# Optimization experiments

Hardware: AMD Instinct MI355X
Metric: run time of the kernel (lower is better)

The kernel has to match this reference:

```python
import jax, jax.numpy as jnp
import numpy as np
from jax import lax

D_MODEL = 1024
EXPAND = 2
D_INNER = EXPAND * D_MODEL          # 2048
HEADDIM = 64
NHEADS = D_INNER // HEADDIM         # 32
D_STATE = 128
D_CONV = 4
NGROUPS = 1
CONV_DIM = D_INNER + 2 * NGROUPS * D_STATE   # 2304
D_IN_PROJ = 2 * D_INNER + 2 * NGROUPS * D_STATE + NHEADS  # 4384
EPS = 1e-5
BSZ, SEQ = 4, 1024


def _layer_norm(x):
    mu = jnp.mean(x, -1, keepdims=True)
    v = jnp.var(x, -1, keepdims=True)
    return (x - mu) * lax.rsqrt(v + EPS)


def _smart_flip(X, mask):
    # reverse only the non-padded prefix of each sequence
    B, L, _ = X.shape
    lengths = jnp.sum(~mask, axis=1)                     # (B,)
    r = jnp.arange(L)[None, :]                           # (1,L)
    pos = jnp.where(r < lengths[:, None], lengths[:, None] - 1 - r, r)
    return jnp.take_along_axis(X, pos[:, :, None], axis=1)


def _mamba2(u, in_proj_w, conv_w, conv_b, dt_bias, A_log, D, norm_w, out_proj_w):
    B, L, _ = u.shape
    zxbcdt = jnp.einsum('bld,ed->ble', u, in_proj_w)     # (B,L,D_IN_PROJ)
    z = zxbcdt[..., :D_INNER]
    xBC = zxbcdt[..., D_INNER:D_INNER + CONV_DIM]
    dt = zxbcdt[..., D_INNER + CONV_DIM:]                # (B,L,H)
    dt = jax.nn.softplus(dt + dt_bias)
    # causal depthwise conv1d over time, then SiLU
    xc = jnp.transpose(xBC, (0, 2, 1))                   # (B,C,L)
    xc = jnp.pad(xc, ((0, 0), (0, 0), (D_CONV - 1, 0)))
    xc = lax.conv_general_dilated(xc, conv_w.reshape(CONV_DIM, 1, D_CONV), (1,), 'VALID',
                                  feature_group_count=CONV_DIM)
    xBC = jax.nn.silu(jnp.transpose(xc + conv_b[None, :, None], (0, 2, 1)))
    x = xBC[..., :D_INNER].reshape(B, L, NHEADS, HEADDIM)
    Bmat = xBC[..., D_INNER:D_INNER + D_STATE]           # (B,L,N)  (ngroups=1)
    Cmat = xBC[..., D_INNER + D_STATE:]                  # (B,L,N)
    A = -jnp.exp(A_log)                                  # (H,)
    dA = jnp.exp(dt * A)                                 # (B,L,H)

    def step(h, inp):
        dA_t, dt_t, x_t, B_t, C_t = inp
        # h: (B,H,P,N)
        h = h * dA_t[:, :, None, None] + (dt_t[:, :, None] * x_t)[..., None] * B_t[:, None, None, :]
        y = jnp.einsum('bhpn,bn->bhp', h, C_t)
        return h, y

    h0 = jnp.zeros((B, NHEADS, HEADDIM, D_STATE), u.dtype)
    xs = (jnp.moveaxis(dA, 1, 0), jnp.moveaxis(dt, 1, 0), jnp.moveaxis(x, 1, 0),
          jnp.moveaxis(Bmat, 1, 0), jnp.moveaxis(Cmat, 1, 0))
    _, ys = lax.scan(step, h0, xs)                       # (L,B,H,P)
    y = jnp.moveaxis(ys, 0, 1) + D[None, None, :, None] * x
    y = y.reshape(B, L, D_INNER)
    g = y * jax.nn.silu(z)                               # gated RMSNorm (norm_before_gate=False)
    y = g * lax.rsqrt(jnp.mean(g * g, -1, keepdims=True) + EPS) * norm_w
    return jnp.einsum('ble,de->bld', y, out_proj_w)


def setup_inputs() -> dict:
    key = jax.random.key(0)
    ks = jax.random.split(key, 16)
    dt_f = jax.random.uniform(ks[4], (NHEADS,), minval=0.001, maxval=0.1)
    dt_r = jax.random.uniform(ks[10], (NHEADS,), minval=0.001, maxval=0.1)
    inv_softplus = lambda d: d + jnp.log(-jnp.expm1(-d))
    return {
        'hidden_states': jax.random.normal(ks[0], (BSZ, SEQ, D_MODEL), jnp.float32),
        'src_key_padding_mask': jnp.zeros((BSZ, SEQ), jnp.bool_),
        'in_proj_w': jax.random.normal(ks[1], (D_IN_PROJ, D_MODEL), jnp.float32) / np.sqrt(D_MODEL),
        'out_proj_w': jax.random.normal(ks[2], (D_MODEL, D_INNER), jnp.float32) / np.sqrt(D_INNER),
        'conv_w_f': jax.random.normal(ks[3], (CONV_DIM, D_CONV), jnp.float32) / np.sqrt(D_CONV),
        'conv_b_f': jnp.zeros((CONV_DIM,), jnp.float32),
        'dt_bias_f': inv_softplus(dt_f),
        'A_log_f': jnp.log(jax.random.uniform(ks[5], (NHEADS,), minval=1.0, maxval=16.0)),
        'D_f': jnp.ones((NHEADS,), jnp.float32),
        'norm_w_f': jnp.ones((D_INNER,), jnp.float32),
        'conv_w_r': jax.random.normal(ks[9], (CONV_DIM, D_CONV), jnp.float32) / np.sqrt(D_CONV),
        'conv_b_r': jnp.zeros((CONV_DIM,), jnp.float32),
        'dt_bias_r': inv_softplus(dt_r),
        'A_log_r': jnp.log(jax.random.uniform(ks[11], (NHEADS,), minval=1.0, maxval=16.0)),
        'D_r': jnp.ones((NHEADS,), jnp.float32),
        'norm_w_r': jnp.ones((D_INNER,), jnp.float32),
    }


def reference(hidden_states, src_key_padding_mask, in_proj_w, out_proj_w,
              conv_w_f, conv_b_f, dt_bias_f, A_log_f, D_f, norm_w_f,
              conv_w_r, conv_b_r, dt_bias_r, A_log_r, D_r, norm_w_r):
    h = _layer_norm(hidden_states)
    out = _mamba2(h, in_proj_w, conv_w_f, conv_b_f, dt_bias_f, A_log_f, D_f, norm_w_f, out_proj_w)
    rev = _smart_flip(h, src_key_padding_mask)
    out_rev = _mamba2(rev, in_proj_w, conv_w_r, conv_b_r, dt_bias_r, A_log_r, D_r, norm_w_r, out_proj_w)
    out_rev = _smart_flip(out_rev, src_key_padding_mask)
    out = (out + out_rev) / 2
    return _layer_norm(out)
```

## Files before the change

### kernel.cpp

```cpp
#include <hip/hip_runtime.h>


#define BSZ 4
#define SEQ 1024
#define DMODEL 1024
#define DINNER 2048
#define NHEADS 32
#define HEADDIM 64
#define DSTATE 128
#define CONVDIM 2304
#define DPROJ 4384
#define DPROJ_PAD 4480
#define NTOK (BSZ*SEQ)
#define EPSF 1e-5f
#define CH 32
#define NCHK (SEQ/CH)

typedef float f32x4 __attribute__((ext_vector_type(4)));
typedef __bf16 bf16x8 __attribute__((ext_vector_type(8)));

__device__ __forceinline__ unsigned short f2bf(float f) {
  unsigned int x = __float_as_uint(f);
  unsigned int r = (x + 0x7fffu + ((x >> 16) & 1u)) >> 16;
  return (unsigned short)r;
}
__device__ __forceinline__ float bf2f(unsigned short u) {
  return __uint_as_float(((unsigned int)u) << 16);
}

__device__ __forceinline__ void async_load16(const void* g, void* l) {
  __builtin_amdgcn_global_load_lds(
      (const __attribute__((address_space(1))) void*)g,
      (__attribute__((address_space(3))) void*)l, 16, 0, 0);
}

#define W1N (DPROJ_PAD * DMODEL)
#define W2N (DMODEL * DINNER)
__global__ void k_convert(const float* __restrict__ w1, const float* __restrict__ w2,
                          unsigned short* __restrict__ o1, unsigned short* __restrict__ o2) {
  int idx = blockIdx.x * 256 + threadIdx.x;
  if (idx < W1N) {
    int row = idx >> 10, col = idx & 1023;
    float v = (row < DPROJ) ? w1[(size_t)row * DMODEL + col] : 0.f;
    o1[idx] = f2bf(v);
  } else {
    int k = idx - W1N;
    o2[k] = f2bf(w2[k]);
  }
}
__global__ void k_lengths(const unsigned char* __restrict__ mask, int* __restrict__ lengths) {
  int b = blockIdx.x, tid = threadIdx.x;
  int cnt = 0;
  for (int k = 0; k < 4; ++k)
    cnt += (mask[(size_t)b * SEQ + tid + k * 256] == 0) ? 1 : 0;
  for (int o = 32; o > 0; o >>= 1) cnt += __shfl_down(cnt, o);
  __shared__ int red[4];
  if ((tid & 63) == 0) red[tid >> 6] = cnt;
  __syncthreads();
  if (tid == 0) lengths[b] = red[0] + red[1] + red[2] + red[3];
}

__global__ __launch_bounds__(256) void k_ln_bf16(const float* __restrict__ in,
                                                 unsigned short* __restrict__ out) {
  int row = blockIdx.x, tid = threadIdx.x;
  float4 v = ((const float4*)(in + (size_t)row * DMODEL))[tid];
  float s = v.x + v.y + v.z + v.w;
  float ss = v.x * v.x + v.y * v.y + v.z * v.z + v.w * v.w;
  for (int o = 32; o > 0; o >>= 1) { s += __shfl_down(s, o); ss += __shfl_down(ss, o); }
  __shared__ float red[8];
  if ((tid & 63) == 0) { red[tid >> 6] = s; red[4 + (tid >> 6)] = ss; }
  __syncthreads();
  s = red[0] + red[1] + red[2] + red[3];
// ... 118 lines not shown
  for (int k = 0; k < 9; ++k) {
    int c = tid + k * 256;
    float4 w4 = *(const float4*)(cw + (size_t)c * 4);
    w0[k] = w4.x; w1[k] = w4.y; w2[k] = w4.z; w3[k] = w4.w;
    bias[k] = cb[c];
    r0[k] = 0.f; r1[k] = 0.f; r2[k] = 0.f;
  }
  auto rowptr = [&](int tt) -> const __bf16* {
    int s = dir ? ((tt < len) ? (len - 1 - tt) : tt) : tt;
    return zxb + ((size_t)b * SEQ + s) * DPROJ_PAD + DINNER;
  };
  if (t0 >= 3) {
    const __bf16* ra = rowptr(t0 - 3);
    const __bf16* rb = rowptr(t0 - 2);
    const __bf16* rc = rowptr(t0 - 1);
#pragma unroll
    for (int k = 0; k < 9; ++k) {
      int c = tid + k * 256;
      r0[k] = (float)ra[c]; r1[k] = (float)rb[c]; r2[k] = (float)rc[c];
    }
  }
  {
    const __bf16* rp = rowptr(t0);
#pragma unroll
    for (int k = 0; k < 9; ++k) r3[k] = (float)rp[tid + k * 256];
  }
  for (int j = 0; j < 16; ++j) {
    float r4[9];
    if (j < 15) {
      const __bf16* rp = rowptr(t0 + j + 1);
#pragma unroll
      for (int k = 0; k < 9; ++k) r4[k] = (float)rp[tid + k * 256];
    }
    __bf16* orow = xb + ((size_t)db * SEQ + t0 + j) * CONVDIM;
#pragma unroll
    for (int k = 0; k < 9; ++k) {
      float acc = bias[k];
      acc = fmaf(w0[k], r0[k], acc);
      acc = fmaf(w1[k], r1[k], acc);
      acc = fmaf(w2[k], r2[k], acc);
      acc = fmaf(w3[k], r3[k], acc);
      float sig = 1.f / (1.f + __expf(-acc));
      orow[tid + k * 256] = (__bf16)(acc * sig);
      r0[k] = r1[k]; r1[k] = r2[k]; r2[k] = r3[k]; r3[k] = r4[k];
    }
  }
}

__global__ __launch_bounds__(256) void k_dtprep(
    const __bf16* __restrict__ zxb,
    const float* __restrict__ dtb_f, const float* __restrict__ dtb_r,
    const float* __restrict__ al_f, const float* __restrict__ al_r,
    const int* __restrict__ lengths, float* __restrict__ ddg) {
  const int task = (blockIdx.x * 256 + threadIdx.x) >> 5;
  const int l32 = threadIdx.x & 31;
  const int chunk = task & 31, hh = (task >> 5) & 31, db = task >> 10;
  const int b = db & 3, dir = db >> 2;
  const int len = lengths[b];
  const float dtbv = (dir ? dtb_r : dtb_f)[hh];
  const float Ah = -__expf((dir ? al_r : al_f)[hh]);
  const int s = chunk * 32 + l32;
  const int sf = dir ? ((s < len) ? (len - 1 - s) : s) : s;
  float raw = (float)zxb[(size_t)(b * SEQ + sf) * DPROJ_PAD + DINNER + CONVDIM + hh] + dtbv;
  float d = (raw > 20.f) ? raw : log1pf(__expf(raw));
  float cum = d;
#pragma unroll
  for (int o = 1; o < 32; o <<= 1) {
    float v = __shfl_up(cum, o, 32);
    if (l32 >= o) cum += v;
  }
  float cum31 = __shfl(cum, 31, 32);
  float* o = ddg + (size_t)task * 128;
  o[l32]      = d;
  o[32 + l32] = Ah * cum;
  o[64 + l32] = d * __expf(Ah * (cum31 - cum));
  o[96 + l32] = __expf(Ah * cum);
}

__global__ __launch_bounds__(256, 2) void k_scan(
    const __bf16* __restrict__ xb, const float* __restrict__ ddg,
    const float* __restrict__ D_f, const float* __restrict__ D_r,
    unsigned short* __restrict__ y) {
  __shared__ __bf16 Crawf[4096];
  __shared__ __bf16 Brawf[4096];
  __shared__ __bf16 Braw2[4096];
  __shared__ __bf16 BTf[4096];
  __shared__ float  ddL[2][128];
  __shared__ __bf16 SL[1024];
  __shared__ __bf16 HL[4][2048];
  __shared__ __bf16 yO[2][32 * 72];

  const int bx = blockIdx.x;
  const int h = bx & 31;
  const int db = bx >> 5;
  const int dir = db >> 2;
  const int tid = threadIdx.x;
  const int lane = tid & 63;
  const int w = tid >> 6;
  const int l15 = lane & 15;
  const int q = lane >> 4;

  const float Dh = (dir ? D_r : D_f)[h];
  const __bf16* xbase = xb + (size_t)db * SEQ * CONVDIM;
  const float* ddbase = ddg + (size_t)bx * NCHK * 128;
  unsigned short* ybase = y + (size_t)db * SEQ * DINNER + h * HEADDIM;

  for (int i = lane; i < 2048; i += 64) HL[w][i] = (__bf16)0.f;
  for (int i = tid; i < 1024; i += 256) SL[i] = (__bf16)0.f;

  f32x4 accH[8] = {};

  auto issue = [&](int c, int nb) {
    const __bf16* xr = xbase + (size_t)c * CH * CONVDIM;
#pragma unroll
    for (int k = 0; k < 2; ++k) {
      const int idx = w * 2 + k;
      const int P = idx * 64 + lane;
      const int tt = P >> 8, kk = (P >> 6) & 3, qq = (P >> 4) & 3, ll = P & 15;
      const __bf16* gB = xr + (size_t)(tt * 16 + ll) * CONVDIM + DINNER + kk * 32 + qq * 8;
      async_load16(gB, &Brawf[idx * 512]);
      async_load16(gB + 128, &Crawf[idx * 512]);
      const int s = P >> 4, n8 = P & 15;
      const __bf16* g2 = xr + (size_t)s * CONVDIM + DINNER + n8 * 8;
      async_load16(g2, &Braw2[idx * 512]);
    }
    if (w == 3 && lane < 32)
      async_load16(ddbase + (size_t)c * 128 + lane * 4, &ddL[nb][0]);
  };

  auto load_xt = [&](int c) {
    bf16x8 v;
    const __bf16* gx = xbase + (size_t)(c * CH + q * 8) * CONVDIM + h * HEADDIM + w * 16 + l15;
#pragma unroll
    for (int j = 0; j < 8; ++j) v[j] = gx[(size_t)j * CONVDIM];
    return v;
  };

  issue(0, 0);
  bf16x8 xt = load_xt(0);
  __syncthreads();

  for (int c = 0; c < NCHK; ++c) {
    const int cb = c & 1, nb = cb ^ 1;

    if (c > 0) {
      const int tf = tid >> 3, p8 = (tid & 7) * 8;
      bf16x8 vy = *(const bf16x8*)&yO[nb][tf * 72 + p8];
      *(bf16x8*)(ybase + (size_t)((c - 1) * CH + tf) * DINNER + p8) = vy;
    }

    {
      const int n = tid & 127, sg = tid >> 7;
#pragma unroll
      for (int e = 0; e < 2; ++e) {
        const int qp = sg * 2 + e;
        bf16x8 v;
#pragma unroll
        for (int j = 0; j < 8; ++j) v[j] = Braw2[(qp * 8 + j) * 128 + n];
        *(bf16x8*)&BTf[((n >> 4) * 64 + qp * 16 + (n & 15)) * 8] = v;
      }
    }

    bf16x8 Cf0[4], Cf1[4];
#pragma unroll
    for (int kk = 0; kk < 4; ++kk) {
      Cf0[kk] = *(const bf16x8*)&Crawf[(kk * 64 + lane) * 8];
      Cf1[kk] = *(const bf16x8*)&Crawf[((4 + kk) * 64 + lane) * 8];
    }
    if (w < 3) {
      const int tt = (w == 0) ? 0 : 1;
      const int ss = (w == 2) ? 1 : 0;
      f32x4 G = {};
#pragma unroll
      for (int kk = 0; kk < 4; ++kk) {
        bf16x8 Bq = *(const bf16x8*)&Brawf[((ss * 4 + kk) * 64 + lane) * 8];
        G = __builtin_amdgcn_mfma_f32_16x16x32_bf16(tt ? Cf1[kk] : Cf0[kk], Bq, G, 0, 0, 0);
      }
      const int sgl = ss * 16 + l15;
      const float sdt = ddL[cb][sgl];
      const float scd = ddL[cb][32 + sgl];
#pragma unroll
      for (int r = 0; r < 4; ++r) {
        const int t0 = q * 4 + r;
        float v = G[r] * sdt * __expf(ddL[cb][32 + tt * 16 + t0] - scd);
        if (tt == ss) {
          if (t0 < l15) v = 0.f;
          else if (t0 == l15) v += Dh;
        }
        SL[(tt * 64 + (ss * 2 + (l15 >> 3)) * 16 + t0) * 8 + (l15 & 7)] = (__bf16)v;
      }
    }
    __syncthreads();

    if (c + 1 < NCHK) issue(c + 1, nb);
    bf16x8 xt_n;
    if (c + 1 < NCHK) xt_n = load_xt(c + 1);

    f32x4 accy0 = {}, accy1 = {};
    {
      bf16x8 S0 = *(const bf16x8*)&SL[(lane) * 8];
      bf16x8 S1 = *(const bf16x8*)&SL[(64 + lane) * 8];
      accy0 = __builtin_amdgcn_mfma_f32_16x16x32_bf16(xt, S0, accy0, 0, 0, 0);
      accy1 = __builtin_amdgcn_mfma_f32_16x16x32_bf16(xt, S1, accy1, 0, 0, 0);
    }
    {
      f32x4 ai0 = {}, ai1 = {};
#pragma unroll
      for (int kk = 0; kk < 4; ++kk) {
        bf16x8 Hf = *(const bf16x8*)&HL[w][(kk * 64 + lane) * 8];
        ai0 = __builtin_amdgcn_mfma_f32_16x16x32_bf16(Hf, Cf0[kk], ai0, 0, 0, 0);
        ai1 = __builtin_amdgcn_mfma_f32_16x16x32_bf16(Hf, Cf1[kk], ai1, 0, 0, 0);
      }
      const float P0 = ddL[cb][96 + l15], P1 = ddL[cb][96 + 16 + l15];
      accy0 = accy0 + ai0 * P0;
      accy1 = accy1 + ai1 * P1;
    }
    {
      const float atot = ddL[cb][96 + 31];
      bf16x8 xw;
#pragma unroll
      for (int j = 0; j < 8; ++j)
        xw[j] = (__bf16)((float)xt[j] * ddL[cb][64 + q * 8 + j]);
#pragma unroll
      for (int nt = 0; nt < 8; ++nt) {
        bf16x8 Bt = *(const bf16x8*)&BTf[(nt * 64 + lane) * 8];
        accH[nt] = accH[nt] * atot;
        accH[nt] = __builtin_amdgcn_mfma_f32_16x16x32_bf16(xw, Bt, accH[nt], 0, 0, 0);
      }
#pragma unroll
      for (int nt = 0; nt < 8; ++nt)
#pragma unroll
        for (int r = 0; r < 4; ++r) {
          const int n = nt * 16 + l15;
          HL[w][((n >> 5) * 64 + ((n & 31) >> 3) * 16 + q * 4 + r) * 8 + (n & 7)] =
              (__bf16)accH[nt][r];
        }
    }
#pragma unroll
    for (int r = 0; r < 4; ++r) {
      const int p = w * 16 + q * 4 + r;
      yO[cb][l15 * 72 + p]        = (__bf16)accy0[r];
      yO[cb][(16 + l15) * 72 + p] = (__bf16)accy1[r];
    }
    xt = xt_n;
    __syncthreads();
  }
  {
    const int tf = tid >> 3, p8 = (tid & 7) * 8;
    bf16x8 vy = *(const bf16x8*)&yO[(NCHK - 1) & 1][tf * 72 + p8];
    *(bf16x8*)(ybase + (size_t)((NCHK - 1) * CH + tf) * DINNER + p8) = vy;
  }
}

__global__ __launch_bounds__(256) void k_gate_combine(
    const __bf16* __restrict__ zxb, const unsigned short* __restrict__ y,
    const float* __restrict__ nw_f, const float* __restrict__ nw_r,
    const int* __restrict__ lengths, unsigned short* __restrict__ comb) {
  const int bx = blockIdx.x;
  const int b = bx >> 10, l = bx & 1023;
  const int tid = threadIdx.x;
  const int len = lengths[b];
  const int pos = (l < len) ? (len - 1 - l) : l;
  const __bf16* z = zxb + (size_t)bx * DPROJ_PAD;
  const unsigned short* yf = y + ((size_t)b * SEQ + l) * DINNER;
  const unsigned short* yr = y + ((size_t)(BSZ + b) * SEQ + pos) * DINNER;

  float gf[8], gr[8];
  float sf = 0.f, sr = 0.f;
#pragma unroll
  for (int k = 0; k < 8; ++k) {
    int c = tid + k * 256;
    float zz = (float)z[c];
    float sz = zz / (1.f + __expf(-zz));
    float vf = bf2f(yf[c]) * sz;
    float vr = bf2f(yr[c]) * sz;
    gf[k] = vf; gr[k] = vr;
    sf += vf * vf; sr += vr * vr;
  }
  for (int o = 32; o > 0; o >>= 1) { sf += __shfl_down(sf, o); sr += __shfl_down(sr, o); }
  __shared__ float red[8];
  if ((tid & 63) == 0) { red[tid >> 6] = sf; red[4 + (tid >> 6)] = sr; }
  __syncthreads();
  sf = red[0] + red[1] + red[2] + red[3];
  sr = red[4] + red[5] + red[6] + red[7];
  float rf = rsqrtf(sf * (1.f / DINNER) + EPSF);
  float rr = rsqrtf(sr * (1.f / DINNER) + EPSF);
#pragma unroll
  for (int k = 0; k < 8; ++k) {
    int c = tid + k * 256;
    float o = 0.5f * (gf[k] * rf * nw_f[c] + gr[k] * rr * nw_r[c]);
    comb[(size_t)bx * DINNER + c] = f2bf(o);
  }
}

extern "C" void kernel_launch(void* const* d_in, const int* in_sizes, int n_in,
                              void* d_out, int out_size, void* d_ws, size_t ws_size,
                              hipStream_t stream) {
  const float* hidden      = (const float*)d_in[0];
  const unsigned char* msk = (const unsigned char*)d_in[1];
  const float* in_proj_w   = (const float*)d_in[2];
  const float* out_proj_w  = (const float*)d_in[3];
  const float* conv_w_f    = (const float*)d_in[4];
  const float* conv_b_f    = (const float*)d_in[5];
  const float* dt_bias_f   = (const float*)d_in[6];
  const float* A_log_f     = (const float*)d_in[7];
  const float* D_f         = (const float*)d_in[8];
  const float* norm_w_f    = (const float*)d_in[9];
  const float* conv_w_r    = (const float*)d_in[10];
  const float* conv_b_r    = (const float*)d_in[11];
  const float* dt_bias_r   = (const float*)d_in[12];
  const float* A_log_r     = (const float*)d_in[13];
  const float* D_r         = (const float*)d_in[14];
  const float* norm_w_r    = (const float*)d_in[15];
  float* outF = (float*)d_out;

  char* ws = (char*)d_ws;
  size_t o_w1b  = 0;
  size_t o_w2b  = o_w1b  + 9175040;
  size_t o_hb   = o_w2b  + 4194304;
  size_t o_zx   = o_hb   + 8388608;
  size_t o_xb   = o_zx   + 36700160;
  size_t o_dd   = o_xb   + 37748736;
  size_t o_y    = o_dd   + 4194304;
  size_t o_comb = o_y    + 33554432;
  size_t o_outp = o_comb + 16777216;
  size_t o_len  = o_outp + 8388608;

  unsigned short* W1b  = (unsigned short*)(ws + o_w1b);
  unsigned short* W2b  = (unsigned short*)(ws + o_w2b);
  unsigned short* hb   = (unsigned short*)(ws + o_hb);
  __bf16*         zxb  = (__bf16*)(ws + o_zx);
  __bf16*         xb   = (__bf16*)(ws + o_xb);
  float*          ddg  = (float*)(ws + o_dd);
  unsigned short* yB   = (unsigned short*)(ws + o_y);
  unsigned short* comb = (unsigned short*)(ws + o_comb);
  unsigned short* outp = (unsigned short*)(ws + o_outp);
  int*            lens = (int*)(ws + o_len);

  k_convert<<<(W1N + W2N) / 256, 256, 0, stream>>>(in_proj_w, out_proj_w, W1b, W2b);
  k_lengths<<<BSZ, 256, 0, stream>>>(msk, lens);

  k_ln_bf16<<<NTOK, 256, 0, stream>>>(hidden, hb);

  k_gemm_bt_h<<<dim3(NTOK / 128, DPROJ_PAD / 128), 256, 0, stream>>>(
      hb, W1b, (unsigned short*)zxb, DMODEL, DMODEL, DMODEL, DPROJ_PAD);

  k_conv<<<2 * BSZ * (SEQ / 16), 256, 0, stream>>>(
      zxb, conv_w_f, conv_b_f, conv_w_r, conv_b_r, lens, xb);

  k_dtprep<<<1024, 256, 0, stream>>>(
      zxb, dt_bias_f, dt_bias_r, A_log_f, A_log_r, lens, ddg);

  k_scan<<<2 * BSZ * NHEADS, 256, 0, stream>>>(xb, ddg, D_f, D_r, yB);

  k_gate_combine<<<NTOK, 256, 0, stream>>>(zxb, yB, norm_w_f, norm_w_r, lens, comb);

  k_gemm_bt_h<<<dim3(NTOK / 128, DMODEL / 128), 256, 0, stream>>>(
      comb, W2b, outp, DINNER, DINNER, DINNER, DMODEL);

  k_ln_out<<<NTOK, 256, 0, stream>>>(outp, outF);

  (void)in_sizes; (void)n_in; (void)out_size; (void)ws_size;
}
```

Before: 312.1 us.

## Deepen scan pipeline: double-buffer B/C/dd loads two chunks ahead, async x loads

The chunked scan kernel now double-buffers the raw B, C and dt-derived data in dynamic shared memory and prefetches two chunks ahead. The per-chunk x tile is now loaded into shared memory asynchronously instead of through strided per-lane global loads. Barriers become explicit s_barrier calls with hand-tuned vmcnt/lgkmcnt waits, and the y writeback moves after the first barrier. The goal is to hide global-load latency in this serial recurrence, but about 94KB of shared memory and the dropped 2-blocks hint may reduce occupancy. The manual wait counts are also fragile.

Result: slower. 321.2 us (+2.9%).

```diff
diff --git a/kernel.cpp b/kernel.cpp
--- a/kernel.cpp
+++ b/kernel.cpp
@@ -267,18 +267,31 @@
   o[96 + l32] = __expf(Ah * cum);
 }
 
-__global__ __launch_bounds__(256, 2) void k_scan(
+#define SM_CRAW 0
+#define SM_BRAW 16384
+#define SM_B2   32768
+#define SM_BTF  49152
+#define SM_XR   57344
+#define SM_DDL  65536
+#define SM_SL   66560
+#define SM_HL   68608
+#define SM_YO   84992
+#define SM_TOTAL 94208
+
+__global__ __launch_bounds__(256) void k_scan(
     const __bf16* __restrict__ xb, const float* __restrict__ ddg,
     const float* __restrict__ D_f, const float* __restrict__ D_r,
     unsigned short* __restrict__ y) {
-  __shared__ __bf16 Crawf[4096];
-  __shared__ __bf16 Brawf[4096];
-  __shared__ __bf16 Braw2[4096];
-  __shared__ __bf16 BTf[4096];
-  __shared__ float  ddL[2][128];
-  __shared__ __bf16 SL[1024];
-  __shared__ __bf16 HL[4][2048];
-  __shared__ __bf16 yO[2][32 * 72];
+  extern __shared__ char smem[];
+  __bf16* const Crawf = (__bf16*)(smem + SM_CRAW);
+  __bf16* const Brawf = (__bf16*)(smem + SM_BRAW);
+  __bf16* const Braw2 = (__bf16*)(smem + SM_B2);
+  __bf16* const BTf   = (__bf16*)(smem + SM_BTF);
+  __bf16* const Xraw  = (__bf16*)(smem + SM_XR);
+  float*  const ddL   = (float*)(smem + SM_DDL);
+  __bf16* const SL    = (__bf16*)(smem + SM_SL);
+  __bf16* const HL    = (__bf16*)(smem + SM_HL);
+  __bf16* const yO    = (__bf16*)(smem + SM_YO);
 
   const int bx = blockIdx.x;
   const int h = bx & 31;
@@ -295,49 +308,48 @@
   const float* ddbase = ddg + (size_t)bx * NCHK * 128;
   unsigned short* ybase = y + (size_t)db * SEQ * DINNER + h * HEADDIM;
 
-  for (int i = lane; i < 2048; i += 64) HL[w][i] = (__bf16)0.f;
-  for (int i = tid; i < 1024; i += 256) SL[i] = (__bf16)0.f;
-
   f32x4 accH[8] = {};
 
-  auto issue = [&](int c, int nb) {
-    const __bf16* xr = xbase + (size_t)c * CH * CONVDIM;
+  auto issue = [&](int c, int buf) {
 #pragma unroll
     for (int k = 0; k < 2; ++k) {
       const int idx = w * 2 + k;
       const int P = idx * 64 + lane;
       const int tt = P >> 8, kk = (P >> 6) & 3, qq = (P >> 4) & 3, ll = P & 15;
+      const __bf16* xr = xbase + (size_t)c * CH * CONVDIM;
       const __bf16* gB = xr + (size_t)(tt * 16 + ll) * CONVDIM + DINNER + kk * 32 + qq * 8;
-      async_load16(gB, &Brawf[idx * 512]);
-      async_load16(gB + 128, &Crawf[idx * 512]);
+      async_load16(gB, Brawf + buf * 4096 + idx * 512);
+      async_load16(gB + 128, Crawf + buf * 4096 + idx * 512);
       const int s = P >> 4, n8 = P & 15;
       const __bf16* g2 = xr + (size_t)s * CONVDIM + DINNER + n8 * 8;
-      async_load16(g2, &Braw2[idx * 512]);
-    }
-    if (w == 3 && lane < 32)
-      async_load16(ddbase + (size_t)c * 128 + lane * 4, &ddL[nb][0]);
+      async_load16(g2, Braw2 + buf * 4096 + idx * 512);
+    }
+    if (lane < 8)
+      async_load16(ddbase + (size_t)c * 128 + w * 32 + lane * 4,
+                   ddL + buf * 128 + w * 32);
   };
 
-  auto load_xt = [&](int c) {
-    bf16x8 v;
-    const __bf16* gx = xbase + (size_t)(c * CH + q * 8) * CONVDIM + h * HEADDIM + w * 16 + l15;
-#pragma unroll
-    for (int j = 0; j < 8; ++j) v[j] = gx[(size_t)j * CONVDIM];
-    return v;
+  auto issue_x = [&](int c, int buf) {
+    const __bf16* gx = xbase + (size_t)(c * CH + w * 8 + (lane >> 3)) * CONVDIM
+                       + h * HEADDIM + (lane & 7) * 8;
+    async_load16(gx, Xraw + buf * 2048 + w * 512);
   };
 
   issue(0, 0);
-  bf16x8 xt = load_xt(0);
-  __syncthreads();
+  __builtin_amdgcn_sched_barrier(0);
+  issue_x(0, 0);
+  __builtin_amdgcn_sched_barrier(0);
+  issue(1, 1);
+  __builtin_amdgcn_sched_barrier(0);
+  for (int i = lane; i < 2048; i += 64) HL[w * 2048 + i] = (__bf16)0.f;
+  for (int i = tid; i < 1024; i += 256) SL[i] = (__bf16)0.f;
+  asm volatile("s_waitcnt vmcnt(8) lgkmcnt(0)" ::: "memory");
+  __builtin_amdgcn_sched_barrier(0);
+  __builtin_amdgcn_s_barrier();
+  __builtin_amdgcn_sched_barrier(0);
 
   for (int c = 0; c < NCHK; ++c) {
     const int cb = c & 1, nb = cb ^ 1;
-
-    if (c > 0) {
-      const int tf = tid >> 3, p8 = (tid & 7) * 8;
-      bf16x8 vy = *(const bf16x8*)&yO[nb][tf * 72 + p8];
-      *(bf16x8*)(ybase + (size_t)((c - 1) * CH + tf) * DINNER + p8) = vy;
-    }
 
     {
       const int n = tid & 127, sg = tid >> 7;
@@ -346,16 +358,16 @@
         const int qp = sg * 2 + e;
         bf16x8 v;
 #pragma unroll
-        for (int j = 0; j < 8; ++j) v[j] = Braw2[(qp * 8 + j) * 128 + n];
-        *(bf16x8*)&BTf[((n >> 4) * 64 + qp * 16 + (n & 15)) * 8] = v;
+        for (int j = 0; j < 8; ++j) v[j] = Braw2[cb * 4096 + (qp * 8 + j) * 128 + n];
+        *(bf16x8*)(BTf + ((n >> 4) * 64 + qp * 16 + (n & 15)) * 8) = v;
       }
     }
 
     bf16x8 Cf0[4], Cf1[4];
 #pragma unroll
     for (int kk = 0; kk < 4; ++kk) {
-      Cf0[kk] = *(const bf16x8*)&Crawf[(kk * 64 + lane) * 8];
-      Cf1[kk] = *(const bf16x8*)&Crawf[((4 + kk) * 64 + lane) * 8];
+      Cf0[kk] = *(const bf16x8*)(Crawf + cb * 4096 + (kk * 64 + lane) * 8);
+      Cf1[kk] = *(const bf16x8*)(Crawf + cb * 4096 + ((4 + kk) * 64 + lane) * 8);
     }
     if (w < 3) {
       const int tt = (w == 0) ? 0 : 1;
@@ -363,16 +375,16 @@
       f32x4 G = {};
 #pragma unroll
       for (int kk = 0; kk < 4; ++kk) {
-        bf16x8 Bq = *(const bf16x8*)&Brawf[((ss * 4 + kk) * 64 + lane) * 8];
+        bf16x8 Bq = *(const bf16x8*)(Brawf + cb * 4096 + ((ss * 4 + kk) * 64 + lane) * 8);
         G = __builtin_amdgcn_mfma_f32_16x16x32_bf16(tt ? Cf1[kk] : Cf0[kk], Bq, G, 0, 0, 0);
       }
       const int sgl = ss * 16 + l15;
-      const float sdt = ddL[cb][sgl];
-      const float scd = ddL[cb][32 + sgl];
+      const float sdt = ddL[cb * 128 + sgl];
+      const float scd = ddL[cb * 128 + 32 + sgl];
 #pragma unroll
       for (int r = 0; r < 4; ++r) {
         const int t0 = q * 4 + r;
-        float v = G[r] * sdt * __expf(ddL[cb][32 + tt * 16 + t0] - scd);
+        float v = G[r] * sdt * __expf(ddL[cb * 128 + 32 + tt * 16 + t0] - scd);
         if (tt == ss) {
           if (t0 < l15) v = 0.f;
           else if (t0 == l15) v += Dh;
@@ -380,16 +392,35 @@
         SL[(tt * 64 + (ss * 2 + (l15 >> 3)) * 16 + t0) * 8 + (l15 & 7)] = (__bf16)v;
       }
     }
-    __syncthreads();
-
-    if (c + 1 < NCHK) issue(c + 1, nb);
-    bf16x8 xt_n;
-    if (c + 1 < NCHK) xt_n = load_xt(c + 1);
+    asm volatile("s_waitcnt lgkmcnt(0)" ::: "memory");
+    __builtin_amdgcn_sched_barrier(0);
+    __builtin_amdgcn_s_barrier();
+    __builtin_amdgcn_sched_barrier(0);
+
+    if (c > 0) {
+      const int tf = tid >> 3, p8 = (tid & 7) * 8;
+      bf16x8 vy = *(const bf16x8*)(yO + nb * 2304 + tf * 72 + p8);
+      *(bf16x8*)(ybase + (size_t)((c - 1) * CH + tf) * DINNER + p8) = vy;
+    }
+    __builtin_amdgcn_sched_barrier(0);
+    if (c == 0)            { asm volatile("s_waitcnt vmcnt(7)" ::: "memory"); }
+    else if (c < NCHK - 1) { asm volatile("s_waitcnt vmcnt(8)" ::: "memory"); }
+    else                   { asm volatile("s_waitcnt vmcnt(1)" ::: "memory"); }
+    __builtin_amdgcn_sched_barrier(0);
+
+    bf16x8 xt;
+    {
+      const __bf16* xr = Xraw + cb * 2048 + w * 16 + l15;
+#pragma unroll
+      for (int j = 0; j < 8; ++j) xt[j] = xr[(q * 8 + j) * 64];
+    }
+    if (c + 1 < NCHK) issue_x(c + 1, nb);
+    __builtin_amdgcn_sched_barrier(0);
 
     f32x4 accy0 = {}, accy1 = {};
     {
-      bf16x8 S0 = *(const bf16x8*)&SL[(lane) * 8];
-      bf16x8 S1 = *(const bf16x8*)&SL[(64 + lane) * 8];
+      bf16x8 S0 = *(const bf16x8*)(SL + lane * 8);
+      bf16x8 S1 = *(const bf16x8*)(SL + (64 + lane) * 8);
       accy0 = __builtin_amdgcn_mfma_f32_16x16x32_bf16(xt, S0, accy0, 0, 0, 0);
       accy1 = __builtin_amdgcn_mfma_f32_16x16x32_bf16(xt, S1, accy1, 0, 0, 0);
     }
@@ -397,23 +428,23 @@
       f32x4 ai0 = {}, ai1 = {};
 #pragma unroll
       for (int kk = 0; kk < 4; ++kk) {
-        bf16x8 Hf = *(const bf16x8*)&HL[w][(kk * 64 + lane) * 8];
+        bf16x8 Hf = *(const bf16x8*)(HL + w * 2048 + (kk * 64 + lane) * 8);
         ai0 = __builtin_amdgcn_mfma_f32_16x16x32_bf16(Hf, Cf0[kk], ai0, 0, 0, 0);
         ai1 = __builtin_amdgcn_mfma_f32_16x16x32_bf16(Hf, Cf1[kk], ai1, 0, 0, 0);
       }
-      const float P0 = ddL[cb][96 + l15], P1 = ddL[cb][96 + 16 + l15];
+      const float P0 = ddL[cb * 128 + 96 + l15], P1 = ddL[cb * 128 + 96 + 16 + l15];
       accy0 = accy0 + ai0 * P0;
       accy1 = accy1 + ai1 * P1;
     }
     {
-      const float atot = ddL[cb][96 + 31];
+      const float atot = ddL[cb * 128 + 96 + 31];
       bf16x8 xw;
 #pragma unroll
       for (int j = 0; j < 8; ++j)
-        xw[j] = (__bf16)((float)xt[j] * ddL[cb][64 + q * 8 + j]);
+        xw[j] = (__bf16)((float)xt[j] * ddL[cb * 128 + 64 + q * 8 + j]);
 #pragma unroll
       for (int nt = 0; nt < 8; ++nt) {
-        bf16x8 Bt = *(const bf16x8*)&BTf[(nt * 64 + lane) * 8];
+        bf16x8 Bt = *(const bf16x8*)(BTf + (nt * 64 + lane) * 8);
         accH[nt] = accH[nt] * atot;
         accH[nt] = __builtin_amdgcn_mfma_f32_16x16x32_bf16(xw, Bt, accH[nt], 0, 0, 0);
       }
@@ -422,22 +453,29 @@
 #pragma unroll
         for (int r = 0; r < 4; ++r) {
           const int n = nt * 16 + l15;
-          HL[w][((n >> 5) * 64 + ((n & 31) >> 3) * 16 + q * 4 + r) * 8 + (n & 7)] =
+          HL[w * 2048 + ((n >> 5) * 64 + ((n & 31) >> 3) * 16 + q * 4 + r) * 8 + (n & 7)] =
               (__bf16)accH[nt][r];
         }
     }
 #pragma unroll
     for (int r = 0; r < 4; ++r) {
       const int p = w * 16 + q * 4 + r;
-      yO[cb][l15 * 72 + p]        = (__bf16)accy0[r];
-      yO[cb][(16 + l15) * 72 + p] = (__bf16)accy1[r];
-    }
-    xt = xt_n;
-    __syncthreads();
+      yO[cb * 2304 + l15 * 72 + p]        = (__bf16)accy0[r];
+      yO[cb * 2304 + (16 + l15) * 72 + p] = (__bf16)accy1[r];
+    }
+    __builtin_amdgcn_sched_barrier(0);
+    if (c + 2 < NCHK) issue(c + 2, cb);
+    __builtin_amdgcn_sched_barrier(0);
+    if (c < NCHK - 2)       { asm volatile("s_waitcnt vmcnt(8) lgkmcnt(0)" ::: "memory"); }
+    else if (c == NCHK - 2) { asm volatile("s_waitcnt vmcnt(1) lgkmcnt(0)" ::: "memory"); }
+    else                    { asm volatile("s_waitcnt lgkmcnt(0)" ::: "memory"); }
+    __builtin_amdgcn_sched_barrier(0);
+    __builtin_amdgcn_s_barrier();
+    __builtin_amdgcn_sched_barrier(0);
   }
   {
     const int tf = tid >> 3, p8 = (tid & 7) * 8;
-    bf16x8 vy = *(const bf16x8*)&yO[(NCHK - 1) & 1][tf * 72 + p8];
+    bf16x8 vy = *(const bf16x8*)(yO + ((NCHK - 1) & 1) * 2304 + tf * 72 + p8);
     *(bf16x8*)(ybase + (size_t)((NCHK - 1) * CH + tf) * DINNER + p8) = vy;
   }
 }
@@ -527,6 +565,13 @@
   unsigned short* outp = (unsigned short*)(ws + o_outp);
   int*            lens = (int*)(ws + o_len);
 
+  static bool s_attr_done = false;
+  if (!s_attr_done) {
+    hipFuncSetAttribute(reinterpret_cast<const void*>(k_scan),
+                        hipFuncAttributeMaxDynamicSharedMemorySize, SM_TOTAL);
+    s_attr_done = true;
+  }
+
   k_convert<<<(W1N + W2N) / 256, 256, 0, stream>>>(in_proj_w, out_proj_w, W1b, W2b);
   k_lengths<<<BSZ, 256, 0, stream>>>(msk, lens);
 
@@ -541,7 +586,7 @@
   k_dtprep<<<1024, 256, 0, stream>>>(
       zxb, dt_bias_f, dt_bias_r, A_log_f, A_log_r, lens, ddg);
 
-  k_scan<<<2 * BSZ * NHEADS, 256, 0, stream>>>(xb, ddg, D_f, D_r, yB);
+  k_scan<<<2 * BSZ * NHEADS, 256, SM_TOTAL, stream>>>(xb, ddg, D_f, D_r, yB);
 
   k_gate_combine<<<NTOK, 256, 0, stream>>>(zxb, yB, norm_w_f, norm_w_r, lens, comb);
 
```

## Transpose scan MFMA operands to vectorize LDS stores and write y directly

Applied to the files above, without the earlier changes.

Swaps the A/B operands of every MFMA in the chunked scan kernel, so each lane's accumulator holds the transposed fragment. That orientation lets S and H be written to LDS as packed 4-element bf16 vectors instead of scattered scalar stores, and lets the decay factors be read as float4. The yO staging buffer and its extra store pass are removed, and y is now written straight from registers to global memory as 2-byte scalar stores. This frees LDS and cuts LDS traffic, at the cost of less coalesced global y writes.

New measurement: 308.6 us. No clear change (-1.1%).

```diff
diff --git a/kernel.cpp b/kernel.cpp
--- a/kernel.cpp
+++ b/kernel.cpp
@@ -18,6 +18,7 @@
 
 typedef float f32x4 __attribute__((ext_vector_type(4)));
 typedef __bf16 bf16x8 __attribute__((ext_vector_type(8)));
+typedef __bf16 bf16x4 __attribute__((ext_vector_type(4)));
 
 __device__ __forceinline__ unsigned short f2bf(float f) {
   unsigned int x = __float_as_uint(f);
@@ -278,7 +279,6 @@
   __shared__ float  ddL[2][128];
   __shared__ __bf16 SL[1024];
   __shared__ __bf16 HL[4][2048];
-  __shared__ __bf16 yO[2][32 * 72];
 
   const int bx = blockIdx.x;
   const int h = bx & 31;
@@ -333,12 +333,6 @@
   for (int c = 0; c < NCHK; ++c) {
     const int cb = c & 1, nb = cb ^ 1;
 
-    if (c > 0) {
-      const int tf = tid >> 3, p8 = (tid & 7) * 8;
-      bf16x8 vy = *(const bf16x8*)&yO[nb][tf * 72 + p8];
-      *(bf16x8*)(ybase + (size_t)((c - 1) * CH + tf) * DINNER + p8) = vy;
-    }
-
     {
       const int n = tid & 127, sg = tid >> 7;
 #pragma unroll
@@ -364,21 +358,23 @@
 #pragma unroll
       for (int kk = 0; kk < 4; ++kk) {
         bf16x8 Bq = *(const bf16x8*)&Brawf[((ss * 4 + kk) * 64 + lane) * 8];
-        G = __builtin_amdgcn_mfma_f32_16x16x32_bf16(tt ? Cf1[kk] : Cf0[kk], Bq, G, 0, 0, 0);
+        G = __builtin_amdgcn_mfma_f32_16x16x32_bf16(Bq, tt ? Cf1[kk] : Cf0[kk], G, 0, 0, 0);
       }
-      const int sgl = ss * 16 + l15;
-      const float sdt = ddL[cb][sgl];
-      const float scd = ddL[cb][32 + sgl];
+      const float cdt = ddL[cb][32 + tt * 16 + l15];
+      f32x4 sdt4 = *(const f32x4*)&ddL[cb][ss * 16 + q * 4];
+      f32x4 cds4 = *(const f32x4*)&ddL[cb][32 + ss * 16 + q * 4];
+      bf16x4 sv;
 #pragma unroll
       for (int r = 0; r < 4; ++r) {
-        const int t0 = q * 4 + r;
-        float v = G[r] * sdt * __expf(ddL[cb][32 + tt * 16 + t0] - scd);
+        const int s0 = q * 4 + r;
+        float v = G[r] * sdt4[r] * __expf(cdt - cds4[r]);
         if (tt == ss) {
-          if (t0 < l15) v = 0.f;
-          else if (t0 == l15) v += Dh;
+          if (l15 < s0) v = 0.f;
+          else if (l15 == s0) v += Dh;
         }
-        SL[(tt * 64 + (ss * 2 + (l15 >> 3)) * 16 + t0) * 8 + (l15 & 7)] = (__bf16)v;
+        sv[r] = (__bf16)v;
       }
+      *(bf16x4*)&SL[tt * 512 + (ss * 2 + (q >> 1)) * 128 + l15 * 8 + (q & 1) * 4] = sv;
     }
     __syncthreads();
 
@@ -388,20 +384,21 @@
 
     f32x4 accy0 = {}, accy1 = {};
     {
-      bf16x8 S0 = *(const bf16x8*)&SL[(lane) * 8];
+      bf16x8 S0 = *(const bf16x8*)&SL[lane * 8];
       bf16x8 S1 = *(const bf16x8*)&SL[(64 + lane) * 8];
-      accy0 = __builtin_amdgcn_mfma_f32_16x16x32_bf16(xt, S0, accy0, 0, 0, 0);
-      accy1 = __builtin_amdgcn_mfma_f32_16x16x32_bf16(xt, S1, accy1, 0, 0, 0);
+      accy0 = __builtin_amdgcn_mfma_f32_16x16x32_bf16(S0, xt, accy0, 0, 0, 0);
+      accy1 = __builtin_amdgcn_mfma_f32_16x16x32_bf16(S1, xt, accy1, 0, 0, 0);
     }
     {
       f32x4 ai0 = {}, ai1 = {};
 #pragma unroll
       for (int kk = 0; kk < 4; ++kk) {
         bf16x8 Hf = *(const bf16x8*)&HL[w][(kk * 64 + lane) * 8];
-        ai0 = __builtin_amdgcn_mfma_f32_16x16x32_bf16(Hf, Cf0[kk], ai0, 0, 0, 0);
-        ai1 = __builtin_amdgcn_mfma_f32_16x16x32_bf16(Hf, Cf1[kk], ai1, 0, 0, 0);
+        ai0 = __builtin_amdgcn_mfma_f32_16x16x32_bf16(Cf0[kk], Hf, ai0, 0, 0, 0);
+        ai1 = __builtin_amdgcn_mfma_f32_16x16x32_bf16(Cf1[kk], Hf, ai1, 0, 0, 0);
       }
-      const float P0 = ddL[cb][96 + l15], P1 = ddL[cb][96 + 16 + l15];
+      f32x4 P0 = *(const f32x4*)&ddL[cb][96 + q * 4];
+      f32x4 P1 = *(const f32x4*)&ddL[cb][96 + 16 + q * 4];
       accy0 = accy0 + ai0 * P0;
       accy1 = accy1 + ai1 * P1;
     }
@@ -415,30 +412,24 @@
       for (int nt = 0; nt < 8; ++nt) {
         bf16x8 Bt = *(const bf16x8*)&BTf[(nt * 64 + lane) * 8];
         accH[nt] = accH[nt] * atot;
-        accH[nt] = __builtin_amdgcn_mfma_f32_16x16x32_bf16(xw, Bt, accH[nt], 0, 0, 0);
+        accH[nt] = __builtin_amdgcn_mfma_f32_16x16x32_bf16(Bt, xw, accH[nt], 0, 0, 0);
       }
 #pragma unroll
-      for (int nt = 0; nt < 8; ++nt)
-#pragma unroll
-        for (int r = 0; r < 4; ++r) {
-          const int n = nt * 16 + l15;
-          HL[w][((n >> 5) * 64 + ((n & 31) >> 3) * 16 + q * 4 + r) * 8 + (n & 7)] =
-              (__bf16)accH[nt][r];
-        }
+      for (int nt = 0; nt < 8; ++nt) {
+        const int n0 = nt * 16 + q * 4;
+        bf16x4 hv;
+#pragma unroll
+        for (int r = 0; r < 4; ++r) hv[r] = (__bf16)accH[nt][r];
+        *(bf16x4*)&HL[w][(n0 >> 5) * 512 + ((n0 >> 3) & 3) * 128 + l15 * 8 + (n0 & 7)] = hv;
+      }
     }
 #pragma unroll
     for (int r = 0; r < 4; ++r) {
-      const int p = w * 16 + q * 4 + r;
-      yO[cb][l15 * 72 + p]        = (__bf16)accy0[r];
-      yO[cb][(16 + l15) * 72 + p] = (__bf16)accy1[r];
+      ybase[(size_t)(c * CH + q * 4 + r) * DINNER + w * 16 + l15] = f2bf(accy0[r]);
+      ybase[(size_t)(c * CH + 16 + q * 4 + r) * DINNER + w * 16 + l15] = f2bf(accy1[r]);
     }
     xt = xt_n;
     __syncthreads();
-  }
-  {
-    const int tf = tid >> 3, p8 = (tid & 7) * 8;
-    bf16x8 vy = *(const bf16x8*)&yO[(NCHK - 1) & 1][tf * 72 + p8];
-    *(bf16x8*)(ybase + (size_t)((NCHK - 1) * CH + tf) * DINNER + p8) = vy;
   }
 }
 
```

## Double scan chunk length to 64 and rework chunked SSD tiling

Applied to the files above, without the earlier changes.

Raises the chunked-scan chunk length from 32 to 64, which halves the number of sequential chunk iterations in k_scan. The intra-chunk score matrix grows to 64x64, and the load, transpose, MFMA and output layouts are reworked to match, with dt prep producing 64-wide cumulative sums. Shared memory moves to a roughly 108 KB dynamic allocation and the two-blocks-per-CU launch bound is dropped, so occupancy may fall. Each chunk also does more intra-chunk quadratic work in exchange for fewer serial state updates and barriers.

After: 329.4 us. +5.6%, slower.

```diff
diff --git a/kernel.cpp b/kernel.cpp
--- a/kernel.cpp
+++ b/kernel.cpp
@@ -13,11 +13,12 @@
 #define DPROJ_PAD 4480
 #define NTOK (BSZ*SEQ)
 #define EPSF 1e-5f
-#define CH 32
+#define CH 64
 #define NCHK (SEQ/CH)
 
 typedef float f32x4 __attribute__((ext_vector_type(4)));
 typedef __bf16 bf16x8 __attribute__((ext_vector_type(8)));
+typedef __bf16 bf16x4 __attribute__((ext_vector_type(4)));
 
 __device__ __forceinline__ unsigned short f2bf(float f) {
   unsigned int x = __float_as_uint(f);
@@ -242,43 +243,54 @@
     const float* __restrict__ dtb_f, const float* __restrict__ dtb_r,
     const float* __restrict__ al_f, const float* __restrict__ al_r,
     const int* __restrict__ lengths, float* __restrict__ ddg) {
-  const int task = (blockIdx.x * 256 + threadIdx.x) >> 5;
-  const int l32 = threadIdx.x & 31;
-  const int chunk = task & 31, hh = (task >> 5) & 31, db = task >> 10;
+  const int task = (blockIdx.x * 256 + threadIdx.x) >> 6;
+  const int l64 = threadIdx.x & 63;
+  const int chunk = task & 15, hh = (task >> 4) & 31, db = task >> 9;
   const int b = db & 3, dir = db >> 2;
   const int len = lengths[b];
   const float dtbv = (dir ? dtb_r : dtb_f)[hh];
   const float Ah = -__expf((dir ? al_r : al_f)[hh]);
-  const int s = chunk * 32 + l32;
+  const int s = chunk * 64 + l64;
   const int sf = dir ? ((s < len) ? (len - 1 - s) : s) : s;
   float raw = (float)zxb[(size_t)(b * SEQ + sf) * DPROJ_PAD + DINNER + CONVDIM + hh] + dtbv;
   float d = (raw > 20.f) ? raw : log1pf(__expf(raw));
   float cum = d;
 #pragma unroll
-  for (int o = 1; o < 32; o <<= 1) {
-    float v = __shfl_up(cum, o, 32);
-    if (l32 >= o) cum += v;
-  }
-  float cum31 = __shfl(cum, 31, 32);
-  float* o = ddg + (size_t)task * 128;
-  o[l32]      = d;
-  o[32 + l32] = Ah * cum;
-  o[64 + l32] = d * __expf(Ah * (cum31 - cum));
-  o[96 + l32] = __expf(Ah * cum);
-}
-
-__global__ __launch_bounds__(256, 2) void k_scan(
+  for (int o = 1; o < 64; o <<= 1) {
+    float v = __shfl_up(cum, o, 64);
+    if (l64 >= o) cum += v;
+  }
+  float cum63 = __shfl(cum, 63, 64);
+  float* o = ddg + (size_t)task * 256;
+  o[l64]       = d;
+  o[64 + l64]  = Ah * cum;
+  o[128 + l64] = d * __expf(Ah * (cum63 - cum));
+  o[192 + l64] = __expf(Ah * cum);
+}
+
+#define SMS_BRAW 0
+#define SMS_CRAW 16384
+#define SMS_B2   32768
+#define SMS_BTF  49152
+#define SMS_DDL  65536
+#define SMS_SL   67584
+#define SMS_HL   75776
+#define SMS_YO   92160
+#define SMS_TOTAL 110592
+
+__global__ __launch_bounds__(256) void k_scan(
     const __bf16* __restrict__ xb, const float* __restrict__ ddg,
     const float* __restrict__ D_f, const float* __restrict__ D_r,
     unsigned short* __restrict__ y) {
-  __shared__ __bf16 Crawf[4096];
-  __shared__ __bf16 Brawf[4096];
-  __shared__ __bf16 Braw2[4096];
-  __shared__ __bf16 BTf[4096];
-  __shared__ float  ddL[2][128];
-  __shared__ __bf16 SL[1024];
-  __shared__ __bf16 HL[4][2048];
-  __shared__ __bf16 yO[2][32 * 72];
+  extern __shared__ char smem[];
+  __bf16* const Brawf = (__bf16*)(smem + SMS_BRAW);
+  __bf16* const Crawf = (__bf16*)(smem + SMS_CRAW);
+  __bf16* const Braw2 = (__bf16*)(smem + SMS_B2);
+  __bf16* const BTf   = (__bf16*)(smem + SMS_BTF);
+  float*  const ddL   = (float*)(smem + SMS_DDL);
+  __bf16* const SL    = (__bf16*)(smem + SMS_SL);
+  __bf16* const HL    = (__bf16*)(smem + SMS_HL);
+  __bf16* const yO    = (__bf16*)(smem + SMS_YO);
 
   const int bx = blockIdx.x;
   const int h = bx & 31;
@@ -292,153 +304,177 @@
 
   const float Dh = (dir ? D_r : D_f)[h];
   const __bf16* xbase = xb + (size_t)db * SEQ * CONVDIM;
-  const float* ddbase = ddg + (size_t)bx * NCHK * 128;
+  const float* ddbase = ddg + (size_t)bx * NCHK * 256;
   unsigned short* ybase = y + (size_t)db * SEQ * DINNER + h * HEADDIM;
 
-  for (int i = lane; i < 2048; i += 64) HL[w][i] = (__bf16)0.f;
-  for (int i = tid; i < 1024; i += 256) SL[i] = (__bf16)0.f;
+  for (int i = lane; i < 2048; i += 64) HL[w * 2048 + i] = (__bf16)0.f;
+  for (int i = tid; i < 4096; i += 256) SL[i] = (__bf16)0.f;
 
   f32x4 accH[8] = {};
 
   auto issue = [&](int c, int nb) {
     const __bf16* xr = xbase + (size_t)c * CH * CONVDIM;
-#pragma unroll
-    for (int k = 0; k < 2; ++k) {
-      const int idx = w * 2 + k;
-      const int P = idx * 64 + lane;
-      const int tt = P >> 8, kk = (P >> 6) & 3, qq = (P >> 4) & 3, ll = P & 15;
-      const __bf16* gB = xr + (size_t)(tt * 16 + ll) * CONVDIM + DINNER + kk * 32 + qq * 8;
-      async_load16(gB, &Brawf[idx * 512]);
-      async_load16(gB + 128, &Crawf[idx * 512]);
-      const int s = P >> 4, n8 = P & 15;
-      const __bf16* g2 = xr + (size_t)s * CONVDIM + DINNER + n8 * 8;
-      async_load16(g2, &Braw2[idx * 512]);
-    }
-    if (w == 3 && lane < 32)
-      async_load16(ddbase + (size_t)c * 128 + lane * 4, &ddL[nb][0]);
+    const int qq8 = q * 8;
+#pragma unroll
+    for (int i = 0; i < 4; ++i) {
+      const __bf16* g = xr + (size_t)(w * 16 + l15) * CONVDIM + DINNER + i * 32 + qq8;
+      async_load16(g, Brawf + (w * 4 + i) * 512);
+      async_load16(g + 128, Crawf + (w * 4 + i) * 512);
+    }
+#pragma unroll
+    for (int j = 0; j < 4; ++j) {
+      const int s = (w * 4 + j) * 4 + q;
+      const __bf16* g2 = xr + (size_t)s * CONVDIM + DINNER + l15 * 8;
+      async_load16(g2, Braw2 + (w * 4 + j) * 512);
+    }
+    if (w == 3)
+      async_load16(ddbase + (size_t)c * 256 + lane * 4, ddL + nb * 256);
   };
 
-  auto load_xt = [&](int c) {
-    bf16x8 v;
+  auto load_xt = [&](int c, bf16x8& lo, bf16x8& hi) {
     const __bf16* gx = xbase + (size_t)(c * CH + q * 8) * CONVDIM + h * HEADDIM + w * 16 + l15;
 #pragma unroll
-    for (int j = 0; j < 8; ++j) v[j] = gx[(size_t)j * CONVDIM];
-    return v;
+    for (int j = 0; j < 8; ++j) {
+      lo[j] = gx[(size_t)j * CONVDIM];
+      hi[j] = gx[(size_t)(32 + j) * CONVDIM];
+    }
   };
 
+  bf16x8 xlo, xhi, xlo_n, xhi_n;
   issue(0, 0);
-  bf16x8 xt = load_xt(0);
+  load_xt(0, xlo, xhi);
   __syncthreads();
 
   for (int c = 0; c < NCHK; ++c) {
     const int cb = c & 1, nb = cb ^ 1;
+    const float* dd = ddL + cb * 256;
 
     if (c > 0) {
-      const int tf = tid >> 3, p8 = (tid & 7) * 8;
-      bf16x8 vy = *(const bf16x8*)&yO[nb][tf * 72 + p8];
-      *(bf16x8*)(ybase + (size_t)((c - 1) * CH + tf) * DINNER + p8) = vy;
-    }
-
+      const int tf = tid >> 2, p16 = (tid & 3) * 16;
+      bf16x8 v0 = *(const bf16x8*)&yO[nb * 4608 + tf * 72 + p16];
+      bf16x8 v1 = *(const bf16x8*)&yO[nb * 4608 + tf * 72 + p16 + 8];
+      unsigned short* yrow = ybase + (size_t)((c - 1) * CH + tf) * DINNER + p16;
+      *(bf16x8*)yrow = v0;
+      *(bf16x8*)(yrow + 8) = v1;
+    }
+
+#pragma unroll
+    for (int k2 = 0; k2 < 4; ++k2) {
+      const int F = tid + k2 * 256;
+      const int t = F >> 6, fl = F & 63;
+      const int nt = t >> 1, sh = t & 1;
+      const int sb = sh * 32 + ((fl >> 4) * 8), nn = nt * 16 + (fl & 15);
+      bf16x8 v;
+#pragma unroll
+      for (int j = 0; j < 8; ++j) v[j] = Braw2[(sb + j) * 128 + nn];
+      *(bf16x8*)&BTf[F * 8] = v;
+    }
+
+    f32x4 accy[4];
     {
-      const int n = tid & 127, sg = tid >> 7;
-#pragma unroll
-      for (int e = 0; e < 2; ++e) {
-        const int qp = sg * 2 + e;
-        bf16x8 v;
-#pragma unroll
-        for (int j = 0; j < 8; ++j) v[j] = Braw2[(qp * 8 + j) * 128 + n];
-        *(bf16x8*)&BTf[((n >> 4) * 64 + qp * 16 + (n & 15)) * 8] = v;
+      bf16x8 Hf[4];
+#pragma unroll
+      for (int kk = 0; kk < 4; ++kk)
+        Hf[kk] = *(const bf16x8*)&HL[w * 2048 + (kk * 64 + lane) * 8];
+#pragma unroll
+      for (int tq = 0; tq < 4; ++tq) {
+        f32x4 ai = {};
+#pragma unroll
+        for (int kk = 0; kk < 4; ++kk) {
+          bf16x8 Cf = *(const bf16x8*)&Crawf[((tq * 4 + kk) * 64 + lane) * 8];
+          ai = __builtin_amdgcn_mfma_f32_16x16x32_bf16(Hf[kk], Cf, ai, 0, 0, 0);
+        }
+        const float P = dd[192 + tq * 16 + l15];
+        accy[tq] = ai * P;
       }
     }
 
-    bf16x8 Cf0[4], Cf1[4];
-#pragma unroll
-    for (int kk = 0; kk < 4; ++kk) {
-      Cf0[kk] = *(const bf16x8*)&Crawf[(kk * 64 + lane) * 8];
-      Cf1[kk] = *(const bf16x8*)&Crawf[((4 + kk) * 64 + lane) * 8];
-    }
-    if (w < 3) {
-      const int tt = (w == 0) ? 0 : 1;
-      const int ss = (w == 2) ? 1 : 0;
-      f32x4 G = {};
-#pragma unroll
-      for (int kk = 0; kk < 4; ++kk) {
-        bf16x8 Bq = *(const bf16x8*)&Brawf[((ss * 4 + kk) * 64 + lane) * 8];
-        G = __builtin_amdgcn_mfma_f32_16x16x32_bf16(tt ? Cf1[kk] : Cf0[kk], Bq, G, 0, 0, 0);
+    {
+      int list[3]; int nT;
+      if (w == 0)      { list[0] = 0x10; list[1] = 0x20; list[2] = 0x30; nT = 3; }
+      else if (w == 1) { list[0] = 0x11; list[1] = 0x21; list[2] = 0x31; nT = 3; }
+      else if (w == 2) { list[0] = 0x22; list[1] = 0x32; list[2] = 0;    nT = 2; }
+      else             { list[0] = 0x33; list[1] = 0x00; list[2] = 0;    nT = 2; }
+      for (int it = 0; it < nT; ++it) {
+        const int tt = list[it] >> 4, ss = list[it] & 15;
+        f32x4 G = {};
+#pragma unroll
+        for (int kk = 0; kk < 4; ++kk) {
+          bf16x8 Cf = *(const bf16x8*)&Crawf[((tt * 4 + kk) * 64 + lane) * 8];
+          bf16x8 Bq = *(const bf16x8*)&Brawf[((ss * 4 + kk) * 64 + lane) * 8];
+          G = __builtin_amdgcn_mfma_f32_16x16x32_bf16(Cf, Bq, G, 0, 0, 0);
+        }
+        const int sg = ss * 16 + l15;
+        const float dts = dd[sg];
+        const float cds = dd[64 + sg];
+        f32x4 cdt4 = *(const f32x4*)&dd[64 + tt * 16 + q * 4];
+#pragma unroll
+        for (int r = 0; r < 4; ++r) {
+          const int t0 = q * 4 + r;
+          float v = G[r] * dts * __expf(cdt4[r] - cds);
+          if (tt == ss) {
+            if (t0 < l15) v = 0.f;
+            else if (t0 == l15) v += Dh;
+          }
+          SL[((tt * 2 + (ss >> 1)) * 64 + ((ss & 1) * 2 + (l15 >> 3)) * 16 + t0) * 8 +
+             (l15 & 7)] = (__bf16)v;
+        }
       }
-      const int sgl = ss * 16 + l15;
-      const float sdt = ddL[cb][sgl];
-      const float scd = ddL[cb][32 + sgl];
-#pragma unroll
-      for (int r = 0; r < 4; ++r) {
-        const int t0 = q * 4 + r;
-        float v = G[r] * sdt * __expf(ddL[cb][32 + tt * 16 + t0] - scd);
-        if (tt == ss) {
-          if (t0 < l15) v = 0.f;
-          else if (t0 == l15) v += Dh;
-        }
-        SL[(tt * 64 + (ss * 2 + (l15 >> 3)) * 16 + t0) * 8 + (l15 & 7)] = (__bf16)v;
+    }
+    __syncthreads();
+
+    if (c + 1 < NCHK) { issue(c + 1, nb); load_xt(c + 1, xlo_n, xhi_n); }
+
+#pragma unroll
+    for (int tq = 0; tq < 4; ++tq) {
+      bf16x8 S0 = *(const bf16x8*)&SL[((tq * 2 + 0) * 64 + lane) * 8];
+      bf16x8 S1 = *(const bf16x8*)&SL[((tq * 2 + 1) * 64 + lane) * 8];
+      accy[tq] = __builtin_amdgcn_mfma_f32_16x16x32_bf16(xlo, S0, accy[tq], 0, 0, 0);
+      accy[tq] = __builtin_amdgcn_mfma_f32_16x16x32_bf16(xhi, S1, accy[tq], 0, 0, 0);
+    }
+
+    {
+      const float atot = dd[192 + 63];
+      bf16x8 xw0, xw1;
+#pragma unroll
+      for (int j = 0; j < 8; ++j) {
+        xw0[j] = (__bf16)((float)xlo[j] * dd[128 + q * 8 + j]);
+        xw1[j] = (__bf16)((float)xhi[j] * dd[128 + 32 + q * 8 + j]);
       }
-    }
-    __syncthreads();
-
-    if (c + 1 < NCHK) issue(c + 1, nb);
-    bf16x8 xt_n;
-    if (c + 1 < NCHK) xt_n = load_xt(c + 1);
-
-    f32x4 accy0 = {}, accy1 = {};
-    {
-      bf16x8 S0 = *(const bf16x8*)&SL[(lane) * 8];
-      bf16x8 S1 = *(const bf16x8*)&SL[(64 + lane) * 8];
-      accy0 = __builtin_amdgcn_mfma_f32_16x16x32_bf16(xt, S0, accy0, 0, 0, 0);
-      accy1 = __builtin_amdgcn_mfma_f32_16x16x32_bf16(xt, S1, accy1, 0, 0, 0);
-    }
-    {
-      f32x4 ai0 = {}, ai1 = {};
-#pragma unroll
-      for (int kk = 0; kk < 4; ++kk) {
-        bf16x8 Hf = *(const bf16x8*)&HL[w][(kk * 64 + lane) * 8];
-        ai0 = __builtin_amdgcn_mfma_f32_16x16x32_bf16(Hf, Cf0[kk], ai0, 0, 0, 0);
-        ai1 = __builtin_amdgcn_mfma_f32_16x16x32_bf16(Hf, Cf1[kk], ai1, 0, 0, 0);
-      }
-      const float P0 = ddL[cb][96 + l15], P1 = ddL[cb][96 + 16 + l15];
-      accy0 = accy0 + ai0 * P0;
-      accy1 = accy1 + ai1 * P1;
-    }
-    {
-      const float atot = ddL[cb][96 + 31];
-      bf16x8 xw;
-#pragma unroll
-      for (int j = 0; j < 8; ++j)
-        xw[j] = (__bf16)((float)xt[j] * ddL[cb][64 + q * 8 + j]);
 #pragma unroll
       for (int nt = 0; nt < 8; ++nt) {
-        bf16x8 Bt = *(const bf16x8*)&BTf[(nt * 64 + lane) * 8];
+        bf16x8 Bt0 = *(const bf16x8*)&BTf[((nt * 2 + 0) * 64 + lane) * 8];
+        bf16x8 Bt1 = *(const bf16x8*)&BTf[((nt * 2 + 1) * 64 + lane) * 8];
         accH[nt] = accH[nt] * atot;
-        accH[nt] = __builtin_amdgcn_mfma_f32_16x16x32_bf16(xw, Bt, accH[nt], 0, 0, 0);
+        accH[nt] = __builtin_amdgcn_mfma_f32_16x16x32_bf16(xw0, Bt0, accH[nt], 0, 0, 0);
+        accH[nt] = __builtin_amdgcn_mfma_f32_16x16x32_bf16(xw1, Bt1, accH[nt], 0, 0, 0);
       }
 #pragma unroll
       for (int nt = 0; nt < 8; ++nt)
 #pragma unroll
         for (int r = 0; r < 4; ++r) {
           const int n = nt * 16 + l15;
-          HL[w][((n >> 5) * 64 + ((n & 31) >> 3) * 16 + q * 4 + r) * 8 + (n & 7)] =
+          HL[w * 2048 + ((n >> 5) * 64 + ((n & 31) >> 3) * 16 + q * 4 + r) * 8 + (n & 7)] =
               (__bf16)accH[nt][r];
         }
     }
 #pragma unroll
-    for (int r = 0; r < 4; ++r) {
-      const int p = w * 16 + q * 4 + r;
-      yO[cb][l15 * 72 + p]        = (__bf16)accy0[r];
-      yO[cb][(16 + l15) * 72 + p] = (__bf16)accy1[r];
-    }
-    xt = xt_n;
+    for (int tq = 0; tq < 4; ++tq)
+#pragma unroll
+      for (int r = 0; r < 4; ++r)
+        yO[cb * 4608 + (tq * 16 + l15) * 72 + w * 16 + q * 4 + r] = (__bf16)accy[tq][r];
+
+    xlo = xlo_n; xhi = xhi_n;
     __syncthreads();
   }
   {
-    const int tf = tid >> 3, p8 = (tid & 7) * 8;
-    bf16x8 vy = *(const bf16x8*)&yO[(NCHK - 1) & 1][tf * 72 + p8];
-    *(bf16x8*)(ybase + (size_t)((NCHK - 1) * CH + tf) * DINNER + p8) = vy;
+    const int tf = tid >> 2, p16 = (tid & 3) * 16;
+    const int lb = (NCHK - 1) & 1;
+    bf16x8 v0 = *(const bf16x8*)&yO[lb * 4608 + tf * 72 + p16];
+    bf16x8 v1 = *(const bf16x8*)&yO[lb * 4608 + tf * 72 + p16 + 8];
+    unsigned short* yrow = ybase + (size_t)((NCHK - 1) * CH + tf) * DINNER + p16;
+    *(bf16x8*)yrow = v0;
+    *(bf16x8*)(yrow + 8) = v1;
   }
 }
 
@@ -527,6 +563,13 @@
   unsigned short* outp = (unsigned short*)(ws + o_outp);
   int*            lens = (int*)(ws + o_len);
 
+  static bool s_attr_done = false;
+  if (!s_attr_done) {
+    hipFuncSetAttribute(reinterpret_cast<const void*>(k_scan),
+                        hipFuncAttributeMaxDynamicSharedMemorySize, SMS_TOTAL);
+    s_attr_done = true;
+  }
+
   k_convert<<<(W1N + W2N) / 256, 256, 0, stream>>>(in_proj_w, out_proj_w, W1b, W2b);
   k_lengths<<<BSZ, 256, 0, stream>>>(msk, lens);
 
@@ -541,7 +584,7 @@
   k_dtprep<<<1024, 256, 0, stream>>>(
       zxb, dt_bias_f, dt_bias_r, A_log_f, A_log_r, lens, ddg);
 
-  k_scan<<<2 * BSZ * NHEADS, 256, 0, stream>>>(xb, ddg, D_f, D_r, yB);
+  k_scan<<<2 * BSZ * NHEADS, 256, SMS_TOTAL, stream>>>(xb, ddg, D_f, D_r, yB);
 
   k_gate_combine<<<NTOK, 256, 0, stream>>>(zxb, yB, norm_w_f, norm_w_r, lens, comb);
 
```
